# Performance work log

Hardware: AMD Instinct MI355X
Metric: run time of the kernel (lower is better)

The kernel has to match this reference:

```python
import jax, jax.numpy as jnp
import numpy as np

B = 16384
L = 128   # l_output_dim
H = 64    # hidden_dim
CTX = 16  # task_ctx_dim
DIMS = [2048, 167, 768, 512, 768, 300]  # RDK, MACCS, MolT5, MolCLR, UniMolV2_84M, GraphMVP
N = len(DIMS)


def setup_inputs() -> dict:
    key = jax.random.key(0)
    ks = jax.random.split(key, 64)
    names = ["x_rdk", "x_maccs", "x_molt5", "x_molclr", "x_unimol", "x_gmvp"]
    inp = {}
    for i, (n, d) in enumerate(zip(names, DIMS)):
        inp[n] = jax.random.normal(ks[i], (B, d), dtype=jnp.float32)
    inp["task_context"] = jax.random.normal(ks[10], (B, CTX), dtype=jnp.float32)
    # per-branch projection Linear(d -> L), stored as [d, L] for x @ W + b
    for i, d in enumerate(DIMS):
        s = 1.0 / np.sqrt(d)
        inp[f"Wp{i}"] = jax.random.uniform(ks[12 + i], (d, L), jnp.float32, -s, s)
        inp[f"bp{i}"] = jax.random.uniform(ks[20 + i], (L,), jnp.float32, -s, s)
    # attention MLP: Linear(L->H), ReLU, Linear(H->1)
    s1 = 1.0 / np.sqrt(L)
    inp["W1"] = jax.random.uniform(ks[30], (L, H), jnp.float32, -s1, s1)
    inp["b1"] = jax.random.uniform(ks[31], (H,), jnp.float32, -s1, s1)
    s2 = 1.0 / np.sqrt(H)
    inp["W2"] = jax.random.uniform(ks[32], (H, 1), jnp.float32, -s2, s2)
    inp["b2"] = jax.random.uniform(ks[33], (1,), jnp.float32, -s2, s2)
    inp["comp_beta"] = jnp.asarray(1.0, dtype=jnp.float32)
    # scalar task gate: Linear(CTX -> N)
    sg = 1.0 / np.sqrt(CTX)
    inp["Wg"] = jax.random.uniform(ks[34], (CTX, N), jnp.float32, -sg, sg)
    inp["bg"] = jax.random.uniform(ks[35], (N,), jnp.float32, -sg, sg)
    return inp


def reference(x_rdk, x_maccs, x_molt5, x_molclr, x_unimol, x_gmvp, task_context,
              Wp0, bp0, Wp1, bp1, Wp2, bp2, Wp3, bp3, Wp4, bp4, Wp5, bp5,
              W1, b1, W2, b2, comp_beta, Wg, bg):
    xs = [x_rdk, x_maccs, x_molt5, x_molclr, x_unimol, x_gmvp]
    Wps = [Wp0, Wp1, Wp2, Wp3, Wp4, Wp5]
    bps = [bp0, bp1, bp2, bp3, bp4, bp5]
    # per-branch projection to L dims
    projs = [x @ W + b for x, W, b in zip(xs, Wps, bps)]
    embeds = jnp.stack(projs, axis=1)  # [B, N, L]
    # validity mask per (sample, branch)
    norms = jnp.linalg.norm(embeds, axis=-1)  # [B, N]
    valid = (~jnp.isnan(embeds).any(axis=-1)) & (norms > 1e-8)  # [B, N]
    # attention MLP score
    h = jax.nn.relu(embeds @ W1 + b1)          # [B, N, H]
    scores = h @ W2 + b2                        # [B, N, 1]
    # cosine complementarity: comp[b, n] = mean_m (1 - cos(proj_n, proj_m))
    normed = embeds / jnp.maximum(norms[..., None], 1e-12)
    cos_sim = jnp.einsum('bnd,bmd->bnm', normed, normed)  # [B, N, N]
    comp_vec = jnp.mean(1.0 - cos_sim, axis=-1, keepdims=True)  # [B, N, 1]
    scores = scores + comp_beta * comp_vec
    # task-aware scalar gate bias
    task_bias = (task_context @ Wg + bg)[:, :, None]  # [B, N, 1]
    scores = scores + task_bias
    # masked softmax over branches
    scores = jnp.where(valid[:, :, None], scores, jnp.float32(-1e9))
    attn_weights = jax.nn.softmax(scores, axis=1)  # [B, N, 1]
    fused = jnp.sum(attn_weights * embeds, axis=1)  # [B, L]
    # dropout is identity (eval mode), sparse_lambda=0 -> sparse_reg omitted
    return fused
```

## Files before the change

### kernel.cpp

```cpp
#include <hip/hip_runtime.h>

typedef _Float16 half8 __attribute__((ext_vector_type(8)));
typedef _Float16 half4 __attribute__((ext_vector_type(4)));
typedef float    floatx4 __attribute__((ext_vector_type(4)));

#define EMB_BYTES 25165824u

extern "C" __global__ __launch_bounds__(256) void k_prep(
    const float* __restrict__ Wp0, const float* __restrict__ Wp1,
    const float* __restrict__ Wp2, const float* __restrict__ Wp3,
    const float* __restrict__ Wp4, const float* __restrict__ Wp5,
    _Float16* __restrict__ Wt)
{
  const int DPAD_[6] = {2048,192,768,512,768,320};
  int j = blockIdx.x*256 + threadIdx.x;
  int i = 0, st = 0, cum = 0;
  #pragma unroll
  for (int q = 0; q < 6; q++){
    int sz = DPAD_[q] << 4;
    if (j >= cum){ i = q; st = cum; }
    cum += sz;
  }
  int local = j - st;
  int kc = local >> 7;
  int c  = local & 127;
  const float* Wp; int d, dpad, woff;
  switch(i){
    case 0:  Wp=Wp0; d=2048; dpad=2048; woff=0;      break;
    case 1:  Wp=Wp1; d=167;  dpad=192;  woff=262144; break;
    case 2:  Wp=Wp2; d=768;  dpad=768;  woff=286720; break;
    case 3:  Wp=Wp3; d=512;  dpad=512;  woff=385024; break;
    case 4:  Wp=Wp4; d=768;  dpad=768;  woff=450560; break;
    default: Wp=Wp5; d=300;  dpad=320;  woff=548864; break;
  }
  half8 h;
  #pragma unroll
  for (int u = 0; u < 8; u++){
    int k = (kc<<3) + u;
    float v = (k < d) ? Wp[(size_t)k*128 + c] : 0.0f;
    h[u] = (_Float16)v;
  }
  *(half8*)(Wt + woff + (size_t)c*dpad + (kc<<3)) = h;
}

extern "C" __global__ __launch_bounds__(256, 4) void k_proj(
    const float* __restrict__ x0, const float* __restrict__ x1,
    const float* __restrict__ x2, const float* __restrict__ x3,
    const float* __restrict__ x4, const float* __restrict__ x5,
    const float* __restrict__ bp0, const float* __restrict__ bp1,
    const float* __restrict__ bp2, const float* __restrict__ bp3,
    const float* __restrict__ bp4, const float* __restrict__ bp5,
    const _Float16* __restrict__ Wt, _Float16* __restrict__ Eo)
{
  __shared__ _Float16 sA[64][260];

  int bl = blockIdx.x;
  int i, mtile;
  if      (bl <  256){ i=0; mtile=bl;      }
  else if (bl <  512){ i=2; mtile=bl-256;  }
  else if (bl <  768){ i=4; mtile=bl-512;  }
  else if (bl < 1024){ i=3; mtile=bl-768;  }
  else if (bl < 1280){ i=5; mtile=bl-1024; }
  else               { i=1; mtile=bl-1280; }

  const float* x; const float* bp; int d, dpad, woff, nch;
  switch(i){
    case 0:  x=x0; bp=bp0; d=2048; dpad=2048; woff=0;      nch=8; break;
    case 1:  x=x1; bp=bp1; d=167;  dpad=192;  woff=262144; nch=1; break;
    case 2:  x=x2; bp=bp2; d=768;  dpad=768;  woff=286720; nch=3; break;
    case 3:  x=x3; bp=bp3; d=512;  dpad=512;  woff=385024; nch=2; break;
    case 4:  x=x4; bp=bp4; d=768;  dpad=768;  woff=450560; nch=3; break;
    default: x=x5; bp=bp5; d=300;  dpad=320;  woff=548864; nch=2; break;
  }
  const _Float16* wt = Wt + woff;
  int row0 = mtile << 6;

  int t = threadIdx.x;
  int lane = t & 63, w = t >> 6;
  int wr = w >> 1, wc = w & 1;
  int l15 = lane & 15, l4 = lane >> 4;

  const _Float16* bbase[4];
  #pragma unroll
  for (int nt = 0; nt < 4; nt++)
    bbase[nt] = wt + (size_t)((wc<<6) + (nt<<4) + l15)*dpad + (l4<<3);

  floatx4 acc[2][4];
  #pragma unroll
  for (int a_ = 0; a_ < 2; a_++)
    #pragma unroll
    for (int b_ = 0; b_ < 4; b_++)
      #pragma unroll
      for (int q = 0; q < 4; q++) acc[a_][b_][q] = 0.0f;

  for (int kc = 0; kc < nch; kc++){
    int kbase = kc << 8;

    half8 bfn[4];
    #pragma unroll
    for (int nt = 0; nt < 4; nt++)
      bfn[nt] = *(const half8*)(bbase[nt] + kbase);

    #pragma unroll
    for (int b = 0; b < 4; b++){
      float4 v[4];
      #pragma unroll
      for (int j = 0; j < 4; j++){
        int r = (w<<4) + (b<<2) + j;
        int k = kbase + (lane<<2);
        const float* p = x + (size_t)(row0 + r)*d + k;
        if (k + 4 <= d) v[j] = *(const float4*)p;
        else {
          v[j].x = (k   < d) ? p[0] : 0.0f;
          v[j].y = (k+1 < d) ? p[1] : 0.0f;
          v[j].z = (k+2 < d) ? p[2] : 0.0f;
          v[j].w = (k+3 < d) ? p[3] : 0.0f;
        }
      }
      #pragma unroll
      for (int j = 0; j < 4; j++){
        int r = (w<<4) + (b<<2) + j;
        half4 h;
        h[0] = (_Float16)v[j].x; h[1] = (_Float16)v[j].y;
        h[2] = (_Float16)v[j].z; h[3] = (_Float16)v[j].w;
        *(half4*)&sA[r][lane<<2] = h;
      }
    }
    __syncthreads();

    int rem = dpad - kbase; if (rem > 256) rem = 256;
    int NS = rem >> 5;
    for (int ks = 0; ks < NS; ks++){
      half8 bfc[4];
      #pragma unroll
      for (int nt = 0; nt < 4; nt++) bfc[nt] = bfn[nt];
      if (ks + 1 < NS){
        #pragma unroll
        for (int nt = 0; nt < 4; nt++)
          bfn[nt] = *(const half8*)(bbase[nt] + kbase + ((ks+1)<<5));
      }
      half8 af0 = *(const half8*)&sA[(wr<<5) + l15     ][(ks<<5)+(l4<<3)];
      half8 af1 = *(const half8*)&sA[(wr<<5) + 16 + l15][(ks<<5)+(l4<<3)];
      #pragma unroll
      for (int nt = 0; nt < 4; nt++)
        acc[0][nt] = __builtin_amdgcn_mfma_f32_16x16x32_f16(af0, bfc[nt], acc[0][nt], 0, 0, 0);
      #pragma unroll
      for (int nt = 0; nt < 4; nt++)
        acc[1][nt] = __builtin_amdgcn_mfma_f32_16x16x32_f16(af1, bfc[nt], acc[1][nt], 0, 0, 0);
    }
    __syncthreads();
  }

  #pragma unroll
  for (int nt = 0; nt < 4; nt++){
    int col = (wc<<6) + (nt<<4) + l15;
    float bv = bp[col];
    #pragma unroll
    for (int mtl = 0; mtl < 2; mtl++){
      int rbase = row0 + (wr<<5) + (mtl<<4) + (l4<<2);
      #pragma unroll
      for (int j = 0; j < 4; j++){
        float v = acc[mtl][nt][j] + bv;
        Eo[(size_t)(rbase + j)*768 + i*128 + col] = (_Float16)v;
      }
    }
  }
}

extern "C" __global__ __launch_bounds__(256) void k_attn(
    const _Float16* __restrict__ E,
    const float* __restrict__ W1, const float* __restrict__ b1,
    const float* __restrict__ W2, const float* __restrict__ b2,
    const float* __restrict__ beta_,
    const float* __restrict__ Wg, const float* __restrict__ bg,
    const float* __restrict__ ctx, float* __restrict__ out)
{
  __shared__ _Float16 eb[192][136];
  __shared__ _Float16 w1t[64][136];
  __shared__ float s_s1[192];
  __shared__ float s_gate[192];

  int t = threadIdx.x;
  int row0 = blockIdx.x << 5;
  int lane = t & 63, wid = t >> 6;
  int l15 = lane & 15, l4 = lane >> 4;

  {
    const _Float16* src = E + (size_t)row0*768;
    #pragma unroll
    for (int jj = 0; jj < 12; jj++){
      int off8 = t + (jj<<8);
      half8 v = *(const half8*)(src + ((size_t)off8<<3));
      int mrow = off8 >> 4; int kq = off8 & 15;
      *(half8*)&eb[mrow][kq<<3] = v;
    }
    #pragma unroll
    for (int jj = 0; jj < 8; jj++){
      int idx4 = t + (jj<<8);
      float4 v = *(const float4*)(W1 + ((size_t)idx4<<2));
      int k = idx4 >> 4; int h4 = (idx4 & 15) << 2;
      w1t[h4  ][k] = (_Float16)v.x;
      w1t[h4+1][k] = (_Float16)v.y;
      w1t[h4+2][k] = (_Float16)v.z;
      w1t[h4+3][k] = (_Float16)v.w;
    }
    if (t < 192){
      int r = t / 6; int n = t - r*6;
      const float* cr = ctx + (size_t)(row0 + r)*16;
      float g = bg[n];
      #pragma unroll
      for (int k = 0; k < 16; k++) g += cr[k] * Wg[k*6 + n];
      s_gate[t] = g;
    }
  }
  __syncthreads();

  {
    floatx4 acc[3][4];
    #pragma unroll
    for (int a_ = 0; a_ < 3; a_++)
      #pragma unroll
      for (int b_ = 0; b_ < 4; b_++)
        #pragma unroll
        for (int q = 0; q < 4; q++) acc[a_][b_][q] = 0.0f;

    #pragma unroll
    for (int ks = 0; ks < 4; ks++){
      half8 bf[4];
      #pragma unroll
      for (int nt = 0; nt < 4; nt++)
        bf[nt] = *(const half8*)&w1t[(nt<<4)+l15][(ks<<5)+(l4<<3)];
      #pragma unroll
      for (int m3 = 0; m3 < 3; m3++){
        half8 af = *(const half8*)&eb[wid*48 + (m3<<4) + l15][(ks<<5)+(l4<<3)];
        #pragma unroll
        for (int nt = 0; nt < 4; nt++)
          acc[m3][nt] = __builtin_amdgcn_mfma_f32_16x16x32_f16(af, bf[nt], acc[m3][nt], 0, 0, 0);
      }
    }
    float vb1[4], vw2[4];
    #pragma unroll
    for (int nt = 0; nt < 4; nt++){
      int col = (nt<<4) + l15;
      vb1[nt] = b1[col]; vw2[nt] = W2[col];
    }
    float b2v = b2[0];
    #pragma unroll
    for (int m3 = 0; m3 < 3; m3++){
      #pragma unroll
      for (int j = 0; j < 4; j++){
        float p = 0.0f;
        #pragma unroll
        for (int nt = 0; nt < 4; nt++){
          float v = acc[m3][nt][j] + vb1[nt];
          v = fmaxf(v, 0.0f);
          p += v * vw2[nt];
        }
        p += __shfl_xor(p, 1); p += __shfl_xor(p, 2);
        p += __shfl_xor(p, 4); p += __shfl_xor(p, 8);
        if (l15 == 0) s_s1[wid*48 + (m3<<4) + (l4<<2) + j] = p + b2v;
      }
    }
  }
  __syncthreads();

  {
    float BETA = beta_[0];
    for (int rr = 0; rr < 8; rr++){
      int lrow = (wid<<3) + rr;
      float e0[6], e1[6];
      #pragma unroll
      for (int n = 0; n < 6; n++){
        e0[n] = (float)eb[lrow*6+n][lane];
        e1[n] = (float)eb[lrow*6+n][64+lane];
      }
      float red[21];
      int c = 0;
      #pragma unroll
      for (int n = 0; n < 6; n++) red[c++] = e0[n]*e0[n] + e1[n]*e1[n];
      #pragma unroll
      for (int n = 0; n < 6; n++){
        #pragma unroll
        for (int m = n+1; m < 6; m++) red[c++] = e0[n]*e0[m] + e1[n]*e1[m];
      }
      #pragma unroll
      for (int q = 0; q < 21; q++){
        float v = red[q];
        v += __shfl_xor(v, 1);  v += __shfl_xor(v, 2);  v += __shfl_xor(v, 4);
        v += __shfl_xor(v, 8);  v += __shfl_xor(v, 16); v += __shfl_xor(v, 32);
        red[q] = v;
      }
      float den[6]; bool val[6];
      #pragma unroll
      for (int n = 0; n < 6; n++){
        val[n] = red[n] > 1e-16f;
        den[n] = fmaxf(sqrtf(red[n]), 1e-12f);
      }
      float csum[6];
      #pragma unroll
      for (int n = 0; n < 6; n++) csum[n] = red[n] / (den[n]*den[n]);
      {
        int cc = 6;
        #pragma unroll
        for (int n = 0; n < 6; n++){
          #pragma unroll
          for (int m = n+1; m < 6; m++){
            float cv = red[cc++] / (den[n]*den[m]);
            csum[n] += cv; csum[m] += cv;
          }
        }
      }
      float sc[6];
      #pragma unroll
      for (int n = 0; n < 6; n++){
        float comp = 1.0f - csum[n]*(1.0f/6.0f);
        float s = s_s1[lrow*6+n] + BETA*comp + s_gate[lrow*6+n];
        sc[n] = val[n] ? s : -1e9f;
      }
      float mx = sc[0];
      #pragma unroll
      for (int n = 1; n < 6; n++) mx = fmaxf(mx, sc[n]);
      float wsum = 0.0f; float w[6];
      #pragma unroll
      for (int n = 0; n < 6; n++){ w[n] = __expf(sc[n]-mx); wsum += w[n]; }
      float inv = 1.0f / wsum;
      float f0 = 0.0f, f1 = 0.0f;
      #pragma unroll
      for (int n = 0; n < 6; n++){
        float wn = w[n]*inv;
        f0 += wn*e0[n]; f1 += wn*e1[n];
      }
      size_t ob = (size_t)(row0 + lrow)*128;
      out[ob + lane]      = f0;
      out[ob + 64 + lane] = f1;
    }
  }
}

extern "C" void kernel_launch(void* const* d_in, const int* in_sizes, int n_in,
                              void* d_out, int out_size, void* d_ws, size_t ws_size,
                              hipStream_t stream)
{
  const float* x0 = (const float*)d_in[0];
  const float* x1 = (const float*)d_in[1];
  const float* x2 = (const float*)d_in[2];
  const float* x3 = (const float*)d_in[3];
  const float* x4 = (const float*)d_in[4];
  const float* x5 = (const float*)d_in[5];
  const float* ctx = (const float*)d_in[6];
  const float* Wp0 = (const float*)d_in[7];  const float* bp0 = (const float*)d_in[8];
  const float* Wp1 = (const float*)d_in[9];  const float* bp1 = (const float*)d_in[10];
  const float* Wp2 = (const float*)d_in[11]; const float* bp2 = (const float*)d_in[12];
  const float* Wp3 = (const float*)d_in[13]; const float* bp3 = (const float*)d_in[14];
  const float* Wp4 = (const float*)d_in[15]; const float* bp4 = (const float*)d_in[16];
  const float* Wp5 = (const float*)d_in[17]; const float* bp5 = (const float*)d_in[18];
  const float* W1 = (const float*)d_in[19];
  const float* b1 = (const float*)d_in[20];
  const float* W2 = (const float*)d_in[21];
  const float* b2 = (const float*)d_in[22];
  const float* beta = (const float*)d_in[23];
  const float* Wg = (const float*)d_in[24];
  const float* bg = (const float*)d_in[25];

  _Float16* ws_e = (_Float16*)d_ws;
  _Float16* Wt   = (_Float16*)((char*)d_ws + EMB_BYTES);
  float* outp = (float*)d_out;

  k_prep<<<288, 256, 0, stream>>>(Wp0, Wp1, Wp2, Wp3, Wp4, Wp5, Wt);
  k_proj<<<1536, 256, 0, stream>>>(x0, x1, x2, x3, x4, x5,
                                   bp0, bp1, bp2, bp3, bp4, bp5, Wt, ws_e);
  k_attn<<<512, 256, 0, stream>>>(ws_e, W1, b1, W2, b2, beta, Wg, bg, ctx, outp);
}
```

Measured before the change: 492.5 us.

## Split projection into per-branch templated kernels with 16-row tiles and swizzled LDS

Replaces the single multi-branch projection kernel with six template-specialised launches, one per branch, each handling a 16-row tile. The whole K dimension of the tile is staged in XOR-swizzled LDS in one pass, and each wave computes 32 output columns with double-buffered weight prefetch. The embedding workspace layout changes from row-interleaved [B,6,128] to branch-major [6,B,128], and the attention kernel's load is updated to match. This drops the runtime branch dispatch and the per-chunk barriers and lets the compiler unroll fully. The cost is much more weight re-reading per row (16-row tiles instead of 64), six separate kernel launches, and large LDS use for the 2048-wide branch.

```diff
diff --git a/kernel.cpp b/kernel.cpp
--- a/kernel.cpp
+++ b/kernel.cpp
@@ -4,6 +4,7 @@
 typedef _Float16 half4 __attribute__((ext_vector_type(4)));
 typedef float    floatx4 __attribute__((ext_vector_type(4)));
 
+#define EMB_ELEMS (16384*128)
 #define EMB_BYTES 25165824u
 
 extern "C" __global__ __launch_bounds__(256) void k_prep(
@@ -43,127 +44,87 @@
   *(half8*)(Wt + woff + (size_t)c*dpad + (kc<<3)) = h;
 }
 
-extern "C" __global__ __launch_bounds__(256, 4) void k_proj(
-    const float* __restrict__ x0, const float* __restrict__ x1,
-    const float* __restrict__ x2, const float* __restrict__ x3,
-    const float* __restrict__ x4, const float* __restrict__ x5,
-    const float* __restrict__ bp0, const float* __restrict__ bp1,
-    const float* __restrict__ bp2, const float* __restrict__ bp3,
-    const float* __restrict__ bp4, const float* __restrict__ bp5,
+template<int I, int D, int DPAD, int WOFF>
+__global__ __launch_bounds__(256) void k_projT(
+    const float* __restrict__ x, const float* __restrict__ bp,
     const _Float16* __restrict__ Wt, _Float16* __restrict__ Eo)
 {
-  __shared__ _Float16 sA[64][260];
-
-  int bl = blockIdx.x;
-  int i, mtile;
-  if      (bl <  256){ i=0; mtile=bl;      }
-  else if (bl <  512){ i=2; mtile=bl-256;  }
-  else if (bl <  768){ i=4; mtile=bl-512;  }
-  else if (bl < 1024){ i=3; mtile=bl-768;  }
-  else if (bl < 1280){ i=5; mtile=bl-1024; }
-  else               { i=1; mtile=bl-1280; }
-
-  const float* x; const float* bp; int d, dpad, woff, nch;
-  switch(i){
-    case 0:  x=x0; bp=bp0; d=2048; dpad=2048; woff=0;      nch=8; break;
-    case 1:  x=x1; bp=bp1; d=167;  dpad=192;  woff=262144; nch=1; break;
-    case 2:  x=x2; bp=bp2; d=768;  dpad=768;  woff=286720; nch=3; break;
-    case 3:  x=x3; bp=bp3; d=512;  dpad=512;  woff=385024; nch=2; break;
-    case 4:  x=x4; bp=bp4; d=768;  dpad=768;  woff=450560; nch=3; break;
-    default: x=x5; bp=bp5; d=300;  dpad=320;  woff=548864; nch=2; break;
-  }
-  const _Float16* wt = Wt + woff;
-  int row0 = mtile << 6;
-
-  int t = threadIdx.x;
-  int lane = t & 63, w = t >> 6;
-  int wr = w >> 1, wc = w & 1;
+  __shared__ _Float16 sA[16][DPAD];
+
+  int t = threadIdx.x, lane = t & 63, w = t >> 6;
   int l15 = lane & 15, l4 = lane >> 4;
-
-  const _Float16* bbase[4];
+  int row0 = blockIdx.x << 4;
+
+  constexpr int NCH = (DPAD + 255) / 256;
+  for (int rr = 0; rr < 4; rr++){
+    int r = (w << 2) + rr;
+    int xsw = (r & 7) << 3;
+    const float* xr = x + (size_t)(row0 + r) * D;
+    if constexpr (D % 256 == 0){
+      float4 v[NCH];
+      #pragma unroll
+      for (int c = 0; c < NCH; c++)
+        v[c] = *(const float4*)(xr + c*256 + (lane << 2));
+      #pragma unroll
+      for (int c = 0; c < NCH; c++){
+        half4 h;
+        h[0]=(_Float16)v[c].x; h[1]=(_Float16)v[c].y;
+        h[2]=(_Float16)v[c].z; h[3]=(_Float16)v[c].w;
+        int k = c*256 + (lane << 2);
+        *(half4*)&sA[r][k ^ xsw] = h;
+      }
+    } else {
+      #pragma unroll
+      for (int c = 0; c < NCH; c++){
+        int k = c*256 + (lane << 2);
+        if (k < DPAD){
+          float a0 = (k   < D) ? xr[k]   : 0.0f;
+          float a1 = (k+1 < D) ? xr[k+1] : 0.0f;
+          float a2 = (k+2 < D) ? xr[k+2] : 0.0f;
+          float a3 = (k+3 < D) ? xr[k+3] : 0.0f;
+          half4 h;
+          h[0]=(_Float16)a0; h[1]=(_Float16)a1; h[2]=(_Float16)a2; h[3]=(_Float16)a3;
+          *(half4*)&sA[r][k ^ xsw] = h;
+        }
+      }
+    }
+  }
+  __syncthreads();
+
+  const _Float16* wt = Wt + WOFF;
+  const _Float16* bb0 = wt + (size_t)((w<<5) + l15)*DPAD + (l4<<3);
+  const _Float16* bb1 = bb0 + (size_t)16*DPAD;
+  constexpr int NS = DPAD >> 5;
+  int asw = (l15 & 7) << 3;
+
+  floatx4 acc0 = {0.f,0.f,0.f,0.f}, acc1 = {0.f,0.f,0.f,0.f};
+  half8 bA0 = *(const half8*)(bb0);
+  half8 bA1 = *(const half8*)(bb1);
+  half8 bB0 = *(const half8*)(bb0 + 32);
+  half8 bB1 = *(const half8*)(bb1 + 32);
+  half8 a0  = *(const half8*)&sA[l15][(l4<<3) ^ asw];
+
+  for (int ks = 0; ks < NS; ks++){
+    half8 bc0 = bA0, bc1 = bA1, ac = a0;
+    bA0 = bB0; bA1 = bB1;
+    if (ks + 2 < NS){
+      bB0 = *(const half8*)(bb0 + ((ks+2)<<5));
+      bB1 = *(const half8*)(bb1 + ((ks+2)<<5));
+    }
+    if (ks + 1 < NS)
+      a0 = *(const half8*)&sA[l15][(((ks+1)<<5) + (l4<<3)) ^ asw];
+    acc0 = __builtin_amdgcn_mfma_f32_16x16x32_f16(ac, bc0, acc0, 0, 0, 0);
+    acc1 = __builtin_amdgcn_mfma_f32_16x16x32_f16(ac, bc1, acc1, 0, 0, 0);
+  }
+
+  _Float16* ep = Eo + (size_t)I*EMB_ELEMS + (size_t)row0*128;
+  int c0 = (w<<5) + l15, c1 = c0 + 16;
+  float bv0 = bp[c0], bv1 = bp[c1];
   #pragma unroll
-  for (int nt = 0; nt < 4; nt++)
-    bbase[nt] = wt + (size_t)((wc<<6) + (nt<<4) + l15)*dpad + (l4<<3);
-
-  floatx4 acc[2][4];
-  #pragma unroll
-  for (int a_ = 0; a_ < 2; a_++)
-    #pragma unroll
-    for (int b_ = 0; b_ < 4; b_++)
-      #pragma unroll
-      for (int q = 0; q < 4; q++) acc[a_][b_][q] = 0.0f;
-
-  for (int kc = 0; kc < nch; kc++){
-    int kbase = kc << 8;
-
-    half8 bfn[4];
-    #pragma unroll
-    for (int nt = 0; nt < 4; nt++)
-      bfn[nt] = *(const half8*)(bbase[nt] + kbase);
-
-    #pragma unroll
-    for (int b = 0; b < 4; b++){
-      float4 v[4];
-      #pragma unroll
-      for (int j = 0; j < 4; j++){
-        int r = (w<<4) + (b<<2) + j;
-        int k = kbase + (lane<<2);
-        const float* p = x + (size_t)(row0 + r)*d + k;
-        if (k + 4 <= d) v[j] = *(const float4*)p;
-        else {
-          v[j].x = (k   < d) ? p[0] : 0.0f;
-          v[j].y = (k+1 < d) ? p[1] : 0.0f;
-          v[j].z = (k+2 < d) ? p[2] : 0.0f;
-          v[j].w = (k+3 < d) ? p[3] : 0.0f;
-        }
-      }
-      #pragma unroll
-      for (int j = 0; j < 4; j++){
-        int r = (w<<4) + (b<<2) + j;
-        half4 h;
-        h[0] = (_Float16)v[j].x; h[1] = (_Float16)v[j].y;
-        h[2] = (_Float16)v[j].z; h[3] = (_Float16)v[j].w;
-        *(half4*)&sA[r][lane<<2] = h;
-      }
-    }
-    __syncthreads();
-
-    int rem = dpad - kbase; if (rem > 256) rem = 256;
-    int NS = rem >> 5;
-    for (int ks = 0; ks < NS; ks++){
-      half8 bfc[4];
-      #pragma unroll
-      for (int nt = 0; nt < 4; nt++) bfc[nt] = bfn[nt];
-      if (ks + 1 < NS){
-        #pragma unroll
-        for (int nt = 0; nt < 4; nt++)
-          bfn[nt] = *(const half8*)(bbase[nt] + kbase + ((ks+1)<<5));
-      }
-      half8 af0 = *(const half8*)&sA[(wr<<5) + l15     ][(ks<<5)+(l4<<3)];
-      half8 af1 = *(const half8*)&sA[(wr<<5) + 16 + l15][(ks<<5)+(l4<<3)];
-      #pragma unroll
-      for (int nt = 0; nt < 4; nt++)
-        acc[0][nt] = __builtin_amdgcn_mfma_f32_16x16x32_f16(af0, bfc[nt], acc[0][nt], 0, 0, 0);
-      #pragma unroll
-      for (int nt = 0; nt < 4; nt++)
-        acc[1][nt] = __builtin_amdgcn_mfma_f32_16x16x32_f16(af1, bfc[nt], acc[1][nt], 0, 0, 0);
-    }
-    __syncthreads();
-  }
-
-  #pragma unroll
-  for (int nt = 0; nt < 4; nt++){
-    int col = (wc<<6) + (nt<<4) + l15;
-    float bv = bp[col];
-    #pragma unroll
-    for (int mtl = 0; mtl < 2; mtl++){
-      int rbase = row0 + (wr<<5) + (mtl<<4) + (l4<<2);
-      #pragma unroll
-      for (int j = 0; j < 4; j++){
-        float v = acc[mtl][nt][j] + bv;
-        Eo[(size_t)(rbase + j)*768 + i*128 + col] = (_Float16)v;
-      }
-    }
+  for (int j = 0; j < 4; j++){
+    int r = (l4<<2) + j;
+    ep[r*128 + c0] = (_Float16)(acc0[j] + bv0);
+    ep[r*128 + c1] = (_Float16)(acc1[j] + bv1);
   }
 }
 
@@ -186,13 +147,16 @@
   int l15 = lane & 15, l4 = lane >> 4;
 
   {
-    const _Float16* src = E + (size_t)row0*768;
-    #pragma unroll
-    for (int jj = 0; jj < 12; jj++){
-      int off8 = t + (jj<<8);
-      half8 v = *(const half8*)(src + ((size_t)off8<<3));
-      int mrow = off8 >> 4; int kq = off8 & 15;
-      *(half8*)&eb[mrow][kq<<3] = v;
+    #pragma unroll
+    for (int n = 0; n < 6; n++){
+      const _Float16* pn = E + (size_t)n*EMB_ELEMS + (size_t)row0*128;
+      #pragma unroll
+      for (int jj = 0; jj < 2; jj++){
+        int off8 = t + (jj<<8);
+        half8 v = *(const half8*)(pn + ((size_t)off8<<3));
+        int r = off8 >> 4; int kq = off8 & 15;
+        *(half8*)&eb[r*6+n][kq<<3] = v;
+      }
     }
     #pragma unroll
     for (int jj = 0; jj < 8; jj++){
@@ -367,7 +331,11 @@
   float* outp = (float*)d_out;
 
   k_prep<<<288, 256, 0, stream>>>(Wp0, Wp1, Wp2, Wp3, Wp4, Wp5, Wt);
-  k_proj<<<1536, 256, 0, stream>>>(x0, x1, x2, x3, x4, x5,
-                                   bp0, bp1, bp2, bp3, bp4, bp5, Wt, ws_e);
+  k_projT<0,2048,2048,     0><<<1024, 256, 0, stream>>>(x0, bp0, Wt, ws_e);
+  k_projT<2, 768, 768,286720><<<1024, 256, 0, stream>>>(x2, bp2, Wt, ws_e);
+  k_projT<4, 768, 768,450560><<<1024, 256, 0, stream>>>(x4, bp4, Wt, ws_e);
+  k_projT<3, 512, 512,385024><<<1024, 256, 0, stream>>>(x3, bp3, Wt, ws_e);
+  k_projT<5, 300, 320,548864><<<1024, 256, 0, stream>>>(x5, bp5, Wt, ws_e);
+  k_projT<1, 167, 192,262144><<<1024, 256, 0, stream>>>(x1, bp1, Wt, ws_e);
   k_attn<<<512, 256, 0, stream>>>(ws_e, W1, b1, W2, b2, beta, Wg, bg, ctx, outp);
 }
```

Measured after the change: 521.9 us. 6.0% more time.
